# Performance work log

Measured on AMD Instinct MI355X. Metric: run time of the kernel, lower is better.

The kernel has to match this reference:

```python
import jax, jax.numpy as jnp
import numpy as np

B, C, H, W = 16, 512, 32, 32
GROUPS = 8
EPS = 1e-5


def setup_inputs() -> dict:
    key = jax.random.key(0)
    ks = jax.random.split(key, 7)
    s = 1.0 / np.sqrt(C)
    return {
        "x": jax.random.normal(ks[0], (B, C, H, W), dtype=jnp.float32),
        "gamma": jnp.ones((C,), dtype=jnp.float32),
        "beta": jnp.zeros((C,), dtype=jnp.float32),
        "w_qkv": jax.random.normal(ks[1], (3 * C, C), dtype=jnp.float32) * s,
        "b_qkv": jnp.zeros((3 * C,), dtype=jnp.float32),
        "w_proj": jax.random.normal(ks[2], (C, C), dtype=jnp.float32) * s,
        "b_proj": jnp.zeros((C,), dtype=jnp.float32),
    }


def group_norm(x, gamma, beta):
    b, c, h, w = x.shape
    xg = x.reshape(b, GROUPS, c // GROUPS, h, w)
    mean = xg.mean(axis=(2, 3, 4), keepdims=True)
    var = xg.var(axis=(2, 3, 4), keepdims=True)
    xn = ((xg - mean) * jax.lax.rsqrt(var + EPS)).reshape(b, c, h, w)
    return xn * gamma[None, :, None, None] + beta[None, :, None, None]


def reference(x, gamma, beta, w_qkv, b_qkv, w_proj, b_proj):
    b, c, h, w = x.shape
    n = h * w
    hn = group_norm(x, gamma, beta)
    # 1x1 conv == channel matmul: [3C, C] x [B, C, N] -> [B, 3C, N]
    qkv = jnp.einsum('oc,bcn->bon', w_qkv, hn.reshape(b, c, n)) + b_qkv[None, :, None]
    q, k, v = jnp.split(qkv, 3, axis=1)  # each [B, C, N]
    scale = c ** (-0.5)
    # scores [B, N, N]: q^T k
    attn = jax.nn.softmax(jnp.einsum('bcn,bcm->bnm', q, k) * scale, axis=-1)
    out = jnp.einsum('bnm,bcm->bcn', attn, v)  # [B, C, N]
    proj = jnp.einsum('oc,bcn->bon', w_proj, out) + b_proj[None, :, None]
    return x + proj.reshape(b, c, h, w)
```

## Files before the change

### kernel.cpp

```cpp
#include <hip/hip_runtime.h>


#define BATCH 16
#define CCH 512
#define NSP 1024
#define EPSV 1e-5f
#define BK 32
#define HT 4096

typedef short bf16x8 __attribute__((ext_vector_type(8)));
typedef float f32x4 __attribute__((ext_vector_type(4)));

__device__ __forceinline__ unsigned short f2bf(float f) {
    unsigned int u = __float_as_uint(f);
    u += 0x7FFF + ((u >> 16) & 1);
    return (unsigned short)(u >> 16);
}

__device__ __forceinline__ void glds16(const void* g, void* l) {
    __builtin_amdgcn_global_load_lds(
        (const __attribute__((address_space(1))) unsigned int*)g,
        (__attribute__((address_space(3))) unsigned int*)l, 16, 0, 0);
}

#define MEMF asm volatile("" ::: "memory")
#define VMW(n) asm volatile("s_waitcnt vmcnt(" #n ")" ::: "memory")

#define XCD_MAP(GX_LOG2, PER, xv, yv, bv)                 \
    const int lin_ = blockIdx.x;                          \
    const int xcd_ = lin_ & 7;                            \
    int slot_ = lin_ >> 3;                                \
    const int hi_ = (slot_ >= (PER)) ? 1 : 0;             \
    const int bv = xcd_ + 8 * hi_;                        \
    slot_ -= hi_ * (PER);                                 \
    const int xv = slot_ & ((1 << (GX_LOG2)) - 1);        \
    const int yv = slot_ >> (GX_LOG2);

__device__ __forceinline__ void gemm128_dbuf(
    const unsigned short* __restrict__ Ag, const unsigned short* __restrict__ Bg,
    int astr, int bstr, int ktot, short* L, f32x4* acc) {
    const int t = threadIdx.x;
    const int w = t >> 6, lane = t & 63;
    const int wr = (w >> 1) * 64, wc = (w & 1) * 64;
    const int fr = lane & 15;
    const int fsw = (((lane >> 4) ^ (fr & 3)) * 8);
    const int r0 = t >> 2;
    const int kc = (((t & 3) ^ (r0 & 3)) * 8);
    const unsigned short* Ap0 = Ag + (size_t)r0 * astr + kc;
    const unsigned short* Ap1 = Ag + (size_t)(r0 + 64) * astr + kc;
    const unsigned short* Bp0 = Bg + (size_t)r0 * bstr + kc;
    const unsigned short* Bp1 = Bg + (size_t)(r0 + 64) * bstr + kc;
    short* lw = L + w * 512;

#define STG(bf, kk) do {                                  \
    short* aw_ = lw + (bf) * (4 * HT);                    \
    short* bw_ = aw_ + 2 * HT;                            \
    glds16(Ap0 + (kk), aw_);                              \
    glds16(Ap1 + (kk), aw_ + 2048);                       \
    glds16(Ap0 + (kk) + 32, aw_ + HT);                    \
    glds16(Ap1 + (kk) + 32, aw_ + HT + 2048);             \
    glds16(Bp0 + (kk), bw_);                              \
    glds16(Bp1 + (kk), bw_ + 2048);                       \
    glds16(Bp0 + (kk) + 32, bw_ + HT);                    \
    glds16(Bp1 + (kk) + 32, bw_ + HT + 2048);             \
  } while (0)

#define CMP(bf) do {                                                        \
    _Pragma("unroll")                                                       \
    for (int h = 0; h < 2; h++) {                                           \
        const short* Ab_ = L + (bf) * (4 * HT) + h * HT;                    \
        const short* Bb_ = Ab_ + 2 * HT;                                    \
        bf16x8 af[4], bfr[4];                                               \
        _Pragma("unroll")                                                   \
        for (int mi = 0; mi < 4; mi++)                                      \
            af[mi] = *(const bf16x8*)(Ab_ + (wr + mi * 16 + fr) * BK + fsw);\
        _Pragma("unroll")                                                   \
        for (int ni = 0; ni < 4; ni++)                                      \
            bfr[ni] = *(const bf16x8*)(Bb_ + (wc + ni * 16 + fr) * BK + fsw);\
        _Pragma("unroll")                                                   \
        for (int mi = 0; mi < 4; mi++)                                      \
            _Pragma("unroll")                                               \
            for (int ni = 0; ni < 4; ni++)                                  \
                acc[mi * 4 + ni] = __builtin_amdgcn_mfma_f32_16x16x32_bf16( \
                    af[mi], bfr[ni], acc[mi * 4 + ni], 0, 0, 0);            \
    } } while (0)

    STG(0, 0);
    for (int k0 = 0; k0 < ktot; k0 += 128) {
        STG(1, k0 + 64);
        VMW(8);
        MEMF; __builtin_amdgcn_s_barrier();
        CMP(0);
        MEMF; __builtin_amdgcn_s_barrier();
        const int kb = (k0 + 128 < ktot) ? k0 + 128 : 0;
        STG(0, kb);
        VMW(8);
        MEMF; __builtin_amdgcn_s_barrier();
        CMP(1);
        MEMF; __builtin_amdgcn_s_barrier();
    }
    VMW(0);
#undef STG
#undef CMP
}

__device__ __forceinline__ void gemm128_sb(
    const unsigned short* __restrict__ Ag, const unsigned short* __restrict__ Bg,
    int astr, int bstr, int ktot, short* Al, short* Bl, f32x4* acc) {
    const int t = threadIdx.x;
    const int w = t >> 6, lane = t & 63;
    const int wr = (w >> 1) * 64, wc = (w & 1) * 64;
    const int fr = lane & 15;
    const int fsw = (((lane >> 4) ^ (fr & 3)) * 8);
    const int r0 = t >> 2;
    const int kc = (((t & 3) ^ (r0 & 3)) * 8);
    const unsigned short* Ap0 = Ag + (size_t)r0 * astr + kc;
    const unsigned short* Ap1 = Ag + (size_t)(r0 + 64) * astr + kc;
    const unsigned short* Bp0 = Bg + (size_t)r0 * bstr + kc;
    const unsigned short* Bp1 = Bg + (size_t)(r0 + 64) * bstr + kc;
    short* Alw = Al + w * 512;
    short* Blw = Bl + w * 512;
    for (int k0 = 0; k0 < ktot; k0 += 64) {
        glds16(Ap0 + k0, Alw);
        glds16(Ap1 + k0, Alw + 2048);
        glds16(Ap0 + k0 + 32, Alw + HT);
        glds16(Ap1 + k0 + 32, Alw + HT + 2048);
        glds16(Bp0 + k0, Blw);
        glds16(Bp1 + k0, Blw + 2048);
        glds16(Bp0 + k0 + 32, Blw + HT);
        glds16(Bp1 + k0 + 32, Blw + HT + 2048);
        __syncthreads();
#pragma unroll
        for (int h = 0; h < 2; h++) {
            const short* Ab = Al + h * HT;
            const short* Bb = Bl + h * HT;
            bf16x8 af[4], bfr[4];
#pragma unroll
            for (int mi = 0; mi < 4; mi++)
                af[mi] = *(const bf16x8*)(Ab + (wr + mi * 16 + fr) * BK + fsw);
#pragma unroll
            for (int ni = 0; ni < 4; ni++)
                bfr[ni] = *(const bf16x8*)(Bb + (wc + ni * 16 + fr) * BK + fsw);
#pragma unroll
            for (int mi = 0; mi < 4; mi++)
#pragma unroll
                for (int ni = 0; ni < 4; ni++)
                    acc[mi * 4 + ni] = __builtin_amdgcn_mfma_f32_16x16x32_bf16(
                        af[mi], bfr[ni], acc[mi * 4 + ni], 0, 0, 0);
        }
        __syncthreads();
    }
}

#define EPI_SETUP()                                          \
    const int t = threadIdx.x, lane = t & 63, w = t >> 6;    \
    const int wr = (w >> 1) * 64, wc = (w & 1) * 64;         \
    const int fr = lane & 15, rr0 = (lane >> 4) * 4;

#define ACC_INIT(acc)                                        \
    f32x4 acc[16];                                           \
    _Pragma("unroll") for (int i = 0; i < 16; i++)           \
        acc[i] = (f32x4){0.f, 0.f, 0.f, 0.f};

__global__ __launch_bounds__(256) void setup_k(
    const float* __restrict__ x, float* __restrict__ stats,
    const float* __restrict__ wa, unsigned short* __restrict__ oa, int na4,
    const float* __restrict__ wb, unsigned short* __restrict__ ob, int nb4,
    float* __restrict__ Lsum, const float* __restrict__ bqv,
    unsigned short* __restrict__ wv_t, float* __restrict__ puv) {
    const int t = threadIdx.x;
    const int bx = blockIdx.x;
    __shared__ float rs[4], rq[4];
    __shared__ __align__(16) unsigned short Tt[64 * 72];
    if (bx < 128) {
        const int bg = bx;
        const float4* xp = (const float4*)(x + (size_t)bg * 65536);
        float s = 0.f, q = 0.f;
#pragma unroll
        for (int i = 0; i < 64; i++) {
            float4 v = xp[t + i * 256];
            s += v.x + v.y + v.z + v.w;
            q += v.x * v.x + v.y * v.y + v.z * v.z + v.w * v.w;
        }
#pragma unroll
        for (int off = 32; off; off >>= 1) {
            s += __shfl_down(s, off);
            q += __shfl_down(q, off);
        }
        const int wave = t >> 6, lane = t & 63;
        if (lane == 0) { rs[wave] = s; rq[wave] = q; }
        __syncthreads();
        if (t == 0) {
            float S = rs[0] + rs[1] + rs[2] + rs[3];
            float Q = rq[0] + rq[1] + rq[2] + rq[3];
            const float inv = 1.f / 65536.f;
            float mean = S * inv;
            float var = Q * inv - mean * mean;
            stats[bg * 2] = mean;
            stats[bg * 2 + 1] = rsqrtf(var + EPSV);
        }
    } else if (bx < 896) {
        int i = (bx - 128) * 256 + t;
        const float* src;
        unsigned short* dst;
        int j;
        if (i < na4) { src = wa; dst = oa; j = i; }
        else { j = i - na4; if (j >= nb4) return; src = wb; dst = ob; }
        float4 v = ((const float4*)src)[j];
        ushort4 o;
        o.x = f2bf(v.x); o.y = f2bf(v.y); o.z = f2bf(v.z); o.w = f2bf(v.w);
        ((ushort4*)dst)[j] = o;
    } else if (bx < 912) {
        int i = (bx - 896) * 256 + t;
        ((float4*)Lsum)[i] = (float4){0.f, 0.f, 0.f, 0.f};
    } else if (bx < 976) {
        const int r = bx - 912;
        const float* src = wa + (size_t)2 * 512 * 512;
        const int to = (r >> 3) * 64, tc = (r & 7) * 64;
        const int ol = t >> 2, cs = t & 3;
#pragma unroll
        for (int j = 0; j < 4; j++) {
            float4 v = *(const float4*)(src + (size_t)(to + ol) * 512 + tc + cs * 16 + j * 4);
            int c = cs * 16 + j * 4;
            Tt[(c + 0) * 72 + ol] = f2bf(v.x);
            Tt[(c + 1) * 72 + ol] = f2bf(v.y);
            Tt[(c + 2) * 72 + ol] = f2bf(v.z);
            Tt[(c + 3) * 72 + ol] = f2bf(v.w);
        }
        __syncthreads();
        const int cl = t >> 2, os = t & 3;
        unsigned short* d = wv_t + (size_t)(tc + cl) * 512 + to + os * 16;
        const unsigned short* s2 = Tt + cl * 72 + os * 16;
        *(uint4*)d = *(const uint4*)s2;
        *(uint4*)(d + 8) = *(const uint4*)(s2 + 8);
    } else {
        const int o = (bx - 976) * 256 + t;
        const float* wr_ = wb + (size_t)o * 512;
        const float* bv = bqv + 1024;
        float s = 0.f;
        for (int vv = 0; vv < 512; vv += 4) {
            s += wr_[vv] * bv[vv] + wr_[vv + 1] * bv[vv + 1]
               + wr_[vv + 2] * bv[vv + 2] + wr_[vv + 3] * bv[vv + 3];
        }
        puv[o] = s;
    }
}

__global__ __launch_bounds__(256) void gn_tr_k(
    const float* __restrict__ x, const float* __restrict__ gamma,
    const float* __restrict__ beta, const float* __restrict__ stats,
    unsigned short* __restrict__ hn_t,
    const unsigned short* __restrict__ wp_bf, const unsigned short* __restrict__ wv_t,
    unsigned short* __restrict__ wpv_bf) {
    __shared__ __align__(16) short SM[4 * HT];
    const int lin = blockIdx.x;
    const int t = threadIdx.x;
    if (lin < 16) {
        const int ot = (lin >> 2) * 128, ct2 = (lin & 3) * 128;
        ACC_INIT(acc);
        gemm128_sb(wp_bf + (size_t)ot * 512, wv_t + (size_t)ct2 * 512,
                   512, 512, 512, SM, SM + 2 * HT, acc);
        EPI_SETUP();
#pragma unroll
        for (int ni = 0; ni < 4; ni++) {
            int col = ct2 + wc + ni * 16 + fr;
#pragma unroll
            for (int mi = 0; mi < 4; mi++) {
                int row = ot + wr + mi * 16 + rr0;
#pragma unroll
                for (int r = 0; r < 4; r++)
                    wpv_bf[(size_t)(row + r) * 512 + col] = f2bf(acc[mi * 4 + ni][r]);
            }
        }
        return;
    }
    const int l2 = lin - 16;
    const int nt = l2 & 15, ct = (l2 >> 4) & 7, b = l2 >> 7;
    unsigned short* T = (unsigned short*)SM;
    const float mean = stats[(b * 8 + ct) * 2];
    const float rstd = stats[(b * 8 + ct) * 2 + 1];
    const int cl = t >> 2, nc = t & 3;
    const int c = ct * 64 + cl;
    const float ga = gamma[c] * rstd;
    const float be = beta[c] - mean * ga;
    const float4* xp = (const float4*)(x + ((size_t)b * CCH + c) * NSP + nt * 64);
#pragma unroll
    for (int j = 0; j < 4; j++) {
        float4 v = xp[nc * 4 + j];
        int n = nc * 16 + j * 4;
        T[(n + 0) * 72 + cl] = f2bf(v.x * ga + be);
        T[(n + 1) * 72 + cl] = f2bf(v.y * ga + be);
        T[(n + 2) * 72 + cl] = f2bf(v.z * ga + be);
        T[(n + 3) * 72 + cl] = f2bf(v.w * ga + be);
    }
    __syncthreads();
    const int nl = t >> 2, cc = t & 3;
    unsigned short* dst = hn_t + ((size_t)b * NSP + nt * 64 + nl) * CCH + ct * 64 + cc * 16;
    const unsigned short* src = T + nl * 72 + cc * 16;
    *(uint4*)dst = *(const uint4*)src;
    *(uint4*)(dst + 8) = *(const uint4*)(src + 8);
}

__global__ __launch_bounds__(256) void gemm_qku_k(
    const unsigned short* __restrict__ hn_t, const unsigned short* __restrict__ wq,
    const float* __restrict__ bq, const unsigned short* __restrict__ wpv_bf,
    const float* __restrict__ puv, unsigned short* __restrict__ QKt,
    unsigned short* __restrict__ Ub) {
    __shared__ __align__(16) short L[8 * HT];
    XCD_MAP(3, 96, xb, y, b);
    const int ntc = xb * 128;
    ACC_INIT(acc);
    if (y < 8) {
        const int mt = y * 128;
        gemm128_dbuf(hn_t + ((size_t)b * NSP + mt) * CCH,
                     wq + (size_t)ntc * CCH, CCH, CCH, CCH, L, acc);
        unsigned short* Ob = QKt + (size_t)b * NSP * 1024;
        EPI_SETUP();
#pragma unroll
        for (int ni = 0; ni < 4; ni++) {
            int col = ntc + wc + ni * 16 + fr;
            float bias = bq[col];
#pragma unroll
            for (int mi = 0; mi < 4; mi++) {
                int row = mt + wr + mi * 16 + rr0;
#pragma unroll
                for (int r = 0; r < 4; r++)
                    Ob[(size_t)(row + r) * 1024 + col] = f2bf(acc[mi * 4 + ni][r] + bias);
            }
        }
    } else {
        const int mt = (y - 8) * 128;
        gemm128_dbuf(wpv_bf + (size_t)mt * 512,
                     hn_t + ((size_t)b * NSP + ntc) * CCH, 512, CCH, 512, L, acc);
        unsigned short* Ob = Ub + (size_t)b * CCH * NSP;
        EPI_SETUP();
#pragma unroll
        for (int mi = 0; mi < 4; mi++) {
            int row = mt + wr + mi * 16 + rr0;
#pragma unroll
            for (int r = 0; r < 4; r++) {
                float bias = puv[row + r];
#pragma unroll
                for (int ni = 0; ni < 4; ni++) {
                    int col = ntc + wc + ni * 16 + fr;
                    Ob[(size_t)(row + r) * NSP + col] = f2bf(acc[mi * 4 + ni][r] + bias);
                }
            }
        }
    }
}

__global__ __launch_bounds__(256) void gemm_scores_k(
    const unsigned short* __restrict__ QKt, unsigned short* __restrict__ expS,
    float* __restrict__ Lsum) {
    __shared__ __align__(16) short L[8 * HT];
    XCD_MAP(3, 64, xb, yb, b);
    const int nt = xb * 128, mt = yb * 128;
    const unsigned short* base = QKt + (size_t)b * NSP * 1024;
    ACC_INIT(acc);
    gemm128_dbuf(base + (size_t)mt * 1024, base + (size_t)nt * 1024 + 512,
                 1024, 1024, 512, L, acc);
    unsigned short* Ob = expS + (size_t)b * NSP * NSP;
    float* Ls = Lsum + (size_t)b * NSP;
    const float scale = 0.044194173824159216f;
    EPI_SETUP();
#pragma unroll
    for (int mi = 0; mi < 4; mi++) {
#pragma unroll
        for (int r = 0; r < 4; r++) {
            const int row = mt + wr + mi * 16 + rr0 + r;
            float rs = 0.f;
#pragma unroll
            for (int ni = 0; ni < 4; ni++) {
                int col = nt + wc + ni * 16 + fr;
                float e = __expf(acc[mi * 4 + ni][r] * scale);
                Ob[(size_t)row * NSP + col] = f2bf(e);
                rs += e;
            }
            rs += __shfl_xor(rs, 1);
            rs += __shfl_xor(rs, 2);
            rs += __shfl_xor(rs, 4);
            rs += __shfl_xor(rs, 8);
            if (fr == 0) atomicAdd(&Ls[row], rs);
        }
    }
}

__global__ __launch_bounds__(256) void gemm_pu_k(
    const unsigned short* __restrict__ Ub, const unsigned short* __restrict__ expS,
    const float* __restrict__ Lsum, const float* __restrict__ x,
    const float* __restrict__ bp, float* __restrict__ out) {
    __shared__ __align__(16) short L[8 * HT];
    XCD_MAP(3, 32, xb, yb, b);
    const int nt = xb * 128, ot = yb * 128;
    ACC_INIT(acc);
    gemm128_dbuf(Ub + ((size_t)b * CCH + ot) * NSP,
                 expS + ((size_t)b * NSP + nt) * NSP, NSP, NSP, NSP, L, acc);
    const float* Ls = Lsum + (size_t)b * NSP;
    const size_t bbase = (size_t)b * CCH * NSP;
    EPI_SETUP();
#pragma unroll
    for (int ni = 0; ni < 4; ni++) {
        int col = nt + wc + ni * 16 + fr;
        float invl = __builtin_amdgcn_rcpf(Ls[col]);
#pragma unroll
        for (int mi = 0; mi < 4; mi++) {
            int row = ot + wr + mi * 16 + rr0;
#pragma unroll
            for (int r = 0; r < 4; r++) {
                size_t idx = bbase + (size_t)(row + r) * NSP + col;
                out[idx] = x[idx] + bp[row + r] + acc[mi * 4 + ni][r] * invl;
            }
        }
    }
}

extern "C" void kernel_launch(void* const* d_in, const int* in_sizes, int n_in,
                              void* d_out, int out_size, void* d_ws, size_t ws_size,
                              hipStream_t stream) {
    const float* x = (const float*)d_in[0];
    const float* gamma = (const float*)d_in[1];
    const float* beta = (const float*)d_in[2];
    const float* w_qkv = (const float*)d_in[3];
    const float* b_qkv = (const float*)d_in[4];
    const float* w_proj = (const float*)d_in[5];
    const float* b_proj = (const float*)d_in[6];
    float* out = (float*)d_out;

    char* ws = (char*)d_ws;
    const size_t MB = 1048576;
    const size_t KB = 1024;
    unsigned short* wqkv_bf = (unsigned short*)ws;
    unsigned short* wproj_bf = (unsigned short*)(ws + 1572864);
    float* stats = (float*)(ws + 2 * MB);
    float* Lsum = (float*)(ws + 2 * MB + 64 * KB);
    float* puv = (float*)(ws + 2 * MB + 128 * KB);
    unsigned short* wv_t = (unsigned short*)(ws + 2 * MB + 256 * KB);
    unsigned short* wpv_bf = (unsigned short*)(ws + 3 * MB);
    unsigned short* hn_t = (unsigned short*)(ws + 4 * MB);
    unsigned short* QKt = (unsigned short*)(ws + 24 * MB);
    unsigned short* Ub = (unsigned short*)(ws + 60 * MB);
    unsigned short* expS = (unsigned short*)(ws + 80 * MB);

    setup_k<<<978, 256, 0, stream>>>(x, stats, w_qkv, wqkv_bf, 131072,
                                     w_proj, wproj_bf, 65536, Lsum, b_qkv,
                                     wv_t, puv);
    gn_tr_k<<<2064, 256, 0, stream>>>(x, gamma, beta, stats, hn_t,
                                      wproj_bf, wv_t, wpv_bf);
    gemm_qku_k<<<1536, 256, 0, stream>>>(hn_t, wqkv_bf, b_qkv, wpv_bf, puv,
                                         QKt, Ub);
    gemm_scores_k<<<1024, 256, 0, stream>>>(QKt, expS, Lsum);
    gemm_pu_k<<<512, 256, 0, stream>>>(Ub, expS, Lsum, x, b_proj, out);
}
```

Measured before the change: 204.6 us.

## Fold Wq^T Wk into one matrix so scores skip separate Q and K projections

Precomputes the 512x512 product Wk^T Wq in bf16 inside gn_tr_k. The main GEMM then produces a single T1 = hn·(Wq^T Wk) instead of separate Q and K, which cuts the qkv GEMM from 1536 to 1024 tiles. The scores GEMM now multiplies T1 by the normalized input directly, and the bias cross-terms are added back as per-row and per-column vectors plus a constant in the exp epilogue. The group-norm statistics pass is also split into 512 partial-sum blocks for more parallelism. The cost is extra weight-prep work, atomics for the bias vectors, and a different bf16 rounding path for the combined matrix.

```diff
diff --git a/kernel.cpp b/kernel.cpp
--- a/kernel.cpp
+++ b/kernel.cpp
@@ -15,6 +15,10 @@
     unsigned int u = __float_as_uint(f);
     u += 0x7FFF + ((u >> 16) & 1);
     return (unsigned short)(u >> 16);
+}
+
+__device__ __forceinline__ float bf2f(unsigned short h) {
+    return __uint_as_float(((unsigned int)h) << 16);
 }
 
 __device__ __forceinline__ void glds16(const void* g, void* l) {
@@ -163,44 +167,41 @@
         acc[i] = (f32x4){0.f, 0.f, 0.f, 0.f};
 
 __global__ __launch_bounds__(256) void setup_k(
-    const float* __restrict__ x, float* __restrict__ stats,
+    const float* __restrict__ x, float* __restrict__ sp,
     const float* __restrict__ wa, unsigned short* __restrict__ oa, int na4,
     const float* __restrict__ wb, unsigned short* __restrict__ ob, int nb4,
     float* __restrict__ Lsum, const float* __restrict__ bqv,
-    unsigned short* __restrict__ wv_t, float* __restrict__ puv) {
+    unsigned short* __restrict__ wv_t, unsigned short* __restrict__ wq_t,
+    unsigned short* __restrict__ wk_t, float* __restrict__ puv,
+    float* __restrict__ wu, float* __restrict__ wv_b, float* __restrict__ c0p) {
     const int t = threadIdx.x;
     const int bx = blockIdx.x;
     __shared__ float rs[4], rq[4];
     __shared__ __align__(16) unsigned short Tt[64 * 72];
-    if (bx < 128) {
-        const int bg = bx;
-        const float4* xp = (const float4*)(x + (size_t)bg * 65536);
-        float s = 0.f, q = 0.f;
-#pragma unroll
-        for (int i = 0; i < 64; i++) {
+    if (bx < 512) {
+        const int bg = bx >> 2, q = bx & 3;
+        const float4* xp = (const float4*)(x + (size_t)bg * 65536 + q * 16384);
+        float s = 0.f, qq = 0.f;
+#pragma unroll
+        for (int i = 0; i < 16; i++) {
             float4 v = xp[t + i * 256];
             s += v.x + v.y + v.z + v.w;
-            q += v.x * v.x + v.y * v.y + v.z * v.z + v.w * v.w;
+            qq += v.x * v.x + v.y * v.y + v.z * v.z + v.w * v.w;
         }
 #pragma unroll
         for (int off = 32; off; off >>= 1) {
             s += __shfl_down(s, off);
-            q += __shfl_down(q, off);
+            qq += __shfl_down(qq, off);
         }
         const int wave = t >> 6, lane = t & 63;
-        if (lane == 0) { rs[wave] = s; rq[wave] = q; }
+        if (lane == 0) { rs[wave] = s; rq[wave] = qq; }
         __syncthreads();
         if (t == 0) {
-            float S = rs[0] + rs[1] + rs[2] + rs[3];
-            float Q = rq[0] + rq[1] + rq[2] + rq[3];
-            const float inv = 1.f / 65536.f;
-            float mean = S * inv;
-            float var = Q * inv - mean * mean;
-            stats[bg * 2] = mean;
-            stats[bg * 2 + 1] = rsqrtf(var + EPSV);
-        }
-    } else if (bx < 896) {
-        int i = (bx - 128) * 256 + t;
+            sp[bx * 2] = rs[0] + rs[1] + rs[2] + rs[3];
+            sp[bx * 2 + 1] = rq[0] + rq[1] + rq[2] + rq[3];
+        }
+    } else if (bx < 1280) {
+        int i = (bx - 512) * 256 + t;
         const float* src;
         unsigned short* dst;
         int j;
@@ -210,13 +211,16 @@
         ushort4 o;
         o.x = f2bf(v.x); o.y = f2bf(v.y); o.z = f2bf(v.z); o.w = f2bf(v.w);
         ((ushort4*)dst)[j] = o;
-    } else if (bx < 912) {
-        int i = (bx - 896) * 256 + t;
+    } else if (bx < 1328) {
+        int i = (bx - 1280) * 256 + t;
         ((float4*)Lsum)[i] = (float4){0.f, 0.f, 0.f, 0.f};
-    } else if (bx < 976) {
-        const int r = bx - 912;
-        const float* src = wa + (size_t)2 * 512 * 512;
-        const int to = (r >> 3) * 64, tc = (r & 7) * 64;
+    } else if (bx < 1520) {
+        const int r = bx - 1328;
+        const int sel = r >> 6;
+        const int wrow = (sel == 0) ? 2 : (sel - 1);
+        const float* src = wa + (size_t)wrow * 512 * 512;
+        unsigned short* dst = (sel == 0) ? wv_t : ((sel == 1) ? wq_t : wk_t);
+        const int to = ((r & 63) >> 3) * 64, tc = ((r & 63) & 7) * 64;
         const int ol = t >> 2, cs = t & 3;
 #pragma unroll
         for (int j = 0; j < 4; j++) {
@@ -229,12 +233,12 @@
         }
         __syncthreads();
         const int cl = t >> 2, os = t & 3;
-        unsigned short* d = wv_t + (size_t)(tc + cl) * 512 + to + os * 16;
+        unsigned short* d = dst + (size_t)(tc + cl) * 512 + to + os * 16;
         const unsigned short* s2 = Tt + cl * 72 + os * 16;
         *(uint4*)d = *(const uint4*)s2;
         *(uint4*)(d + 8) = *(const uint4*)(s2 + 8);
-    } else {
-        const int o = (bx - 976) * 256 + t;
+    } else if (bx < 1522) {
+        const int o = (bx - 1520) * 256 + t;
         const float* wr_ = wb + (size_t)o * 512;
         const float* bv = bqv + 1024;
         float s = 0.f;
@@ -243,15 +247,35 @@
                + wr_[vv + 2] * bv[vv + 2] + wr_[vv + 3] * bv[vv + 3];
         }
         puv[o] = s;
+    } else if (bx < 1526) {
+        const int r = bx - 1522;
+        const int isv = r >> 1;
+        const int c = (r & 1) * 256 + t;
+        const float* src = wa + (size_t)isv * 512 * 512;
+        const float* bsr = bqv + (isv ? 0 : 512);
+        float s = 0.f;
+        for (int o = 0; o < 512; o++) s += src[(size_t)o * 512 + c] * bsr[o];
+        (isv ? wv_b : wu)[c] = s;
+    } else {
+        float s = bqv[t] * bqv[512 + t] + bqv[256 + t] * bqv[768 + t];
+#pragma unroll
+        for (int off = 32; off; off >>= 1) s += __shfl_down(s, off);
+        if ((t & 63) == 0) rs[t >> 6] = s;
+        __syncthreads();
+        if (t == 0) c0p[0] = rs[0] + rs[1] + rs[2] + rs[3];
     }
 }
 
 __global__ __launch_bounds__(256) void gn_tr_k(
     const float* __restrict__ x, const float* __restrict__ gamma,
-    const float* __restrict__ beta, const float* __restrict__ stats,
+    const float* __restrict__ beta, const float* __restrict__ sp,
     unsigned short* __restrict__ hn_t,
     const unsigned short* __restrict__ wp_bf, const unsigned short* __restrict__ wv_t,
-    unsigned short* __restrict__ wpv_bf) {
+    unsigned short* __restrict__ wpv_bf,
+    const unsigned short* __restrict__ wk_t, const unsigned short* __restrict__ wq_t,
+    unsigned short* __restrict__ wqkb,
+    const float* __restrict__ wu, const float* __restrict__ wv_b,
+    float* __restrict__ u, float* __restrict__ v) {
     __shared__ __align__(16) short SM[4 * HT];
     const int lin = blockIdx.x;
     const int t = threadIdx.x;
@@ -274,11 +298,39 @@
         }
         return;
     }
-    const int l2 = lin - 16;
+    if (lin < 32) {
+        const int r2 = lin - 16;
+        const int jt = (r2 >> 2) * 128, ct2 = (r2 & 3) * 128;
+        ACC_INIT(acc);
+        gemm128_sb(wk_t + (size_t)jt * 512, wq_t + (size_t)ct2 * 512,
+                   512, 512, 512, SM, SM + 2 * HT, acc);
+        EPI_SETUP();
+#pragma unroll
+        for (int ni = 0; ni < 4; ni++) {
+            int col = ct2 + wc + ni * 16 + fr;
+#pragma unroll
+            for (int mi = 0; mi < 4; mi++) {
+                int row = jt + wr + mi * 16 + rr0;
+#pragma unroll
+                for (int r = 0; r < 4; r++)
+                    wqkb[(size_t)(row + r) * 512 + col] = f2bf(acc[mi * 4 + ni][r]);
+            }
+        }
+        return;
+    }
+    const int l2 = lin - 32;
     const int nt = l2 & 15, ct = (l2 >> 4) & 7, b = l2 >> 7;
     unsigned short* T = (unsigned short*)SM;
-    const float mean = stats[(b * 8 + ct) * 2];
-    const float rstd = stats[(b * 8 + ct) * 2 + 1];
+    const int bg = b * 8 + ct;
+    float S = 0.f, Q = 0.f;
+#pragma unroll
+    for (int qq = 0; qq < 4; qq++) {
+        S += sp[(bg * 4 + qq) * 2];
+        Q += sp[(bg * 4 + qq) * 2 + 1];
+    }
+    const float inv = 1.f / 65536.f;
+    const float mean = S * inv;
+    const float rstd = rsqrtf(Q * inv - mean * mean + EPSV);
     const int cl = t >> 2, nc = t & 3;
     const int c = ct * 64 + cl;
     const float ga = gamma[c] * rstd;
@@ -286,12 +338,12 @@
     const float4* xp = (const float4*)(x + ((size_t)b * CCH + c) * NSP + nt * 64);
 #pragma unroll
     for (int j = 0; j < 4; j++) {
-        float4 v = xp[nc * 4 + j];
+        float4 vx = xp[nc * 4 + j];
         int n = nc * 16 + j * 4;
-        T[(n + 0) * 72 + cl] = f2bf(v.x * ga + be);
-        T[(n + 1) * 72 + cl] = f2bf(v.y * ga + be);
-        T[(n + 2) * 72 + cl] = f2bf(v.z * ga + be);
-        T[(n + 3) * 72 + cl] = f2bf(v.w * ga + be);
+        T[(n + 0) * 72 + cl] = f2bf(vx.x * ga + be);
+        T[(n + 1) * 72 + cl] = f2bf(vx.y * ga + be);
+        T[(n + 2) * 72 + cl] = f2bf(vx.z * ga + be);
+        T[(n + 3) * 72 + cl] = f2bf(vx.w * ga + be);
     }
     __syncthreads();
     const int nl = t >> 2, cc = t & 3;
@@ -299,44 +351,60 @@
     const unsigned short* src = T + nl * 72 + cc * 16;
     *(uint4*)dst = *(const uint4*)src;
     *(uint4*)(dst + 8) = *(const uint4*)(src + 8);
+    float pu = 0.f, pv = 0.f;
+    const int cbase = ct * 64 + cc * 16;
+#pragma unroll
+    for (int j = 0; j < 16; j++) {
+        float hv = bf2f(src[j]);
+        pu += hv * wu[cbase + j];
+        pv += hv * wv_b[cbase + j];
+    }
+    pu += __shfl_xor(pu, 1); pu += __shfl_xor(pu, 2);
+    pv += __shfl_xor(pv, 1); pv += __shfl_xor(pv, 2);
+    if (cc == 0) {
+        atomicAdd(&u[(size_t)b * NSP + nt * 64 + nl], pu);
+        atomicAdd(&v[(size_t)b * NSP + nt * 64 + nl], pv);
+    }
 }
 
 __global__ __launch_bounds__(256) void gemm_qku_k(
-    const unsigned short* __restrict__ hn_t, const unsigned short* __restrict__ wq,
-    const float* __restrict__ bq, const unsigned short* __restrict__ wpv_bf,
-    const float* __restrict__ puv, unsigned short* __restrict__ QKt,
-    unsigned short* __restrict__ Ub) {
+    const unsigned short* __restrict__ hn_t, const unsigned short* __restrict__ wqkb,
+    const unsigned short* __restrict__ wpv_bf, const float* __restrict__ puv,
+    unsigned short* __restrict__ T1, unsigned short* __restrict__ Ub) {
     __shared__ __align__(16) short L[8 * HT];
-    XCD_MAP(3, 96, xb, y, b);
-    const int ntc = xb * 128;
+    const int lin = blockIdx.x, xcd = lin & 7;
+    int slot = lin >> 3;
+    const int hi = (slot >= 64) ? 1 : 0;
+    const int b = xcd + 8 * hi;
+    slot -= hi * 64;
     ACC_INIT(acc);
-    if (y < 8) {
-        const int mt = y * 128;
+    if (slot < 32) {
+        const int mt = (slot >> 2) * 128, jt = (slot & 3) * 128;
         gemm128_dbuf(hn_t + ((size_t)b * NSP + mt) * CCH,
-                     wq + (size_t)ntc * CCH, CCH, CCH, CCH, L, acc);
-        unsigned short* Ob = QKt + (size_t)b * NSP * 1024;
+                     wqkb + (size_t)jt * 512, CCH, 512, CCH, L, acc);
+        unsigned short* Ob = T1 + (size_t)b * NSP * 512;
         EPI_SETUP();
 #pragma unroll
         for (int ni = 0; ni < 4; ni++) {
-            int col = ntc + wc + ni * 16 + fr;
-            float bias = bq[col];
+            int col = jt + wc + ni * 16 + fr;
 #pragma unroll
             for (int mi = 0; mi < 4; mi++) {
                 int row = mt + wr + mi * 16 + rr0;
 #pragma unroll
                 for (int r = 0; r < 4; r++)
-                    Ob[(size_t)(row + r) * 1024 + col] = f2bf(acc[mi * 4 + ni][r] + bias);
+                    Ob[(size_t)(row + r) * 512 + col] = f2bf(acc[mi * 4 + ni][r]);
             }
         }
     } else {
-        const int mt = (y - 8) * 128;
-        gemm128_dbuf(wpv_bf + (size_t)mt * 512,
+        const int s2 = slot - 32;
+        const int ot = (s2 >> 3) * 128, ntc = (s2 & 7) * 128;
+        gemm128_dbuf(wpv_bf + (size_t)ot * 512,
                      hn_t + ((size_t)b * NSP + ntc) * CCH, 512, CCH, 512, L, acc);
         unsigned short* Ob = Ub + (size_t)b * CCH * NSP;
         EPI_SETUP();
 #pragma unroll
         for (int mi = 0; mi < 4; mi++) {
-            int row = mt + wr + mi * 16 + rr0;
+            int row = ot + wr + mi * 16 + rr0;
 #pragma unroll
             for (int r = 0; r < 4; r++) {
                 float bias = puv[row + r];
@@ -351,17 +419,21 @@
 }
 
 __global__ __launch_bounds__(256) void gemm_scores_k(
-    const unsigned short* __restrict__ QKt, unsigned short* __restrict__ expS,
-    float* __restrict__ Lsum) {
+    const unsigned short* __restrict__ T1, const unsigned short* __restrict__ hn_t,
+    unsigned short* __restrict__ expS, float* __restrict__ Lsum,
+    const float* __restrict__ u, const float* __restrict__ v,
+    const float* __restrict__ c0p) {
     __shared__ __align__(16) short L[8 * HT];
     XCD_MAP(3, 64, xb, yb, b);
     const int nt = xb * 128, mt = yb * 128;
-    const unsigned short* base = QKt + (size_t)b * NSP * 1024;
     ACC_INIT(acc);
-    gemm128_dbuf(base + (size_t)mt * 1024, base + (size_t)nt * 1024 + 512,
-                 1024, 1024, 512, L, acc);
+    gemm128_dbuf(T1 + ((size_t)b * NSP + mt) * 512,
+                 hn_t + ((size_t)b * NSP + nt) * CCH, 512, CCH, 512, L, acc);
     unsigned short* Ob = expS + (size_t)b * NSP * NSP;
     float* Ls = Lsum + (size_t)b * NSP;
+    const float* ua = u + (size_t)b * NSP;
+    const float* va = v + (size_t)b * NSP;
+    const float c0v = c0p[0];
     const float scale = 0.044194173824159216f;
     EPI_SETUP();
 #pragma unroll
@@ -369,11 +441,12 @@
 #pragma unroll
         for (int r = 0; r < 4; r++) {
             const int row = mt + wr + mi * 16 + rr0 + r;
+            const float ur = ua[row] + c0v;
             float rs = 0.f;
 #pragma unroll
             for (int ni = 0; ni < 4; ni++) {
                 int col = nt + wc + ni * 16 + fr;
-                float e = __expf(acc[mi * 4 + ni][r] * scale);
+                float e = __expf((acc[mi * 4 + ni][r] + ur + va[col]) * scale);
                 Ob[(size_t)row * NSP + col] = f2bf(e);
                 rs += e;
             }
@@ -432,23 +505,31 @@
     const size_t KB = 1024;
     unsigned short* wqkv_bf = (unsigned short*)ws;
     unsigned short* wproj_bf = (unsigned short*)(ws + 1572864);
-    float* stats = (float*)(ws + 2 * MB);
+    float* sp = (float*)(ws + 2 * MB);
     float* Lsum = (float*)(ws + 2 * MB + 64 * KB);
-    float* puv = (float*)(ws + 2 * MB + 128 * KB);
-    unsigned short* wv_t = (unsigned short*)(ws + 2 * MB + 256 * KB);
-    unsigned short* wpv_bf = (unsigned short*)(ws + 3 * MB);
+    float* u = (float*)(ws + 2 * MB + 128 * KB);
+    float* v = (float*)(ws + 2 * MB + 192 * KB);
+    float* puv = (float*)(ws + 2 * MB + 256 * KB);
+    float* wu = (float*)(ws + 2 * MB + 260 * KB);
+    float* wv_b = (float*)(ws + 2 * MB + 264 * KB);
+    float* c0p = (float*)(ws + 2 * MB + 268 * KB);
+    unsigned short* wv_t = (unsigned short*)(ws + 2 * MB + 512 * KB);
+    unsigned short* wq_t = (unsigned short*)(ws + 3 * MB);
+    unsigned short* wk_t = (unsigned short*)(ws + 3 * MB + 512 * KB);
     unsigned short* hn_t = (unsigned short*)(ws + 4 * MB);
-    unsigned short* QKt = (unsigned short*)(ws + 24 * MB);
+    unsigned short* T1 = (unsigned short*)(ws + 24 * MB);
     unsigned short* Ub = (unsigned short*)(ws + 60 * MB);
     unsigned short* expS = (unsigned short*)(ws + 80 * MB);
-
-    setup_k<<<978, 256, 0, stream>>>(x, stats, w_qkv, wqkv_bf, 131072,
-                                     w_proj, wproj_bf, 65536, Lsum, b_qkv,
-                                     wv_t, puv);
-    gn_tr_k<<<2064, 256, 0, stream>>>(x, gamma, beta, stats, hn_t,
-                                      wproj_bf, wv_t, wpv_bf);
-    gemm_qku_k<<<1536, 256, 0, stream>>>(hn_t, wqkv_bf, b_qkv, wpv_bf, puv,
-                                         QKt, Ub);
-    gemm_scores_k<<<1024, 256, 0, stream>>>(QKt, expS, Lsum);
+    unsigned short* wpv_bf = (unsigned short*)(ws + 114 * MB);
+    unsigned short* wqkb = (unsigned short*)(ws + 115 * MB);
+
+    setup_k<<<1527, 256, 0, stream>>>(x, sp, w_qkv, wqkv_bf, 131072,
+                                      w_proj, wproj_bf, 65536, Lsum, b_qkv,
+                                      wv_t, wq_t, wk_t, puv, wu, wv_b, c0p);
+    gn_tr_k<<<2080, 256, 0, stream>>>(x, gamma, beta, sp, hn_t,
+                                      wproj_bf, wv_t, wpv_bf,
+                                      wk_t, wq_t, wqkb, wu, wv_b, u, v);
+    gemm_qku_k<<<1024, 256, 0, stream>>>(hn_t, wqkb, wpv_bf, puv, T1, Ub);
+    gemm_scores_k<<<1024, 256, 0, stream>>>(T1, hn_t, expS, Lsum, u, v, c0p);
     gemm_pu_k<<<512, 256, 0, stream>>>(Ub, expS, Lsum, x, b_proj, out);
 }
```

After: 208.2 us. No clear change (+1.8%).

## Split GroupNorm stats into partial blocks and halve final GEMM tile height

Applied to the files above, without the earlier changes.

The stats reduction now uses four blocks per group, each writing partial sum and sum-of-squares; gn_tr_k combines them into mean and rstd. The final P·U GEMM switches from 128x128 tiles to 64x128 tiles with a new double-buffered 64-row GEMM routine, doubling its grid from 512 to 1024 blocks. Both changes aim to raise parallelism and CU occupancy on small grids. The cost is less data reuse per tile in the final GEMM and an extra small reduction in the normalization kernel.

```diff
diff --git a/kernel.cpp b/kernel.cpp
--- a/kernel.cpp
+++ b/kernel.cpp
@@ -95,6 +95,70 @@
         const int kb = (k0 + 128 < ktot) ? k0 + 128 : 0;
         STG(0, kb);
         VMW(8);
+        MEMF; __builtin_amdgcn_s_barrier();
+        CMP(1);
+        MEMF; __builtin_amdgcn_s_barrier();
+    }
+    VMW(0);
+#undef STG
+#undef CMP
+}
+
+__device__ __forceinline__ void gemm64_d64(
+    const unsigned short* __restrict__ Ag, const unsigned short* __restrict__ Bg,
+    int astr, int bstr, int ktot, short* L, f32x4* acc) {
+    const int t = threadIdx.x;
+    const int w = t >> 6, lane = t & 63;
+    const int wc = w * 32;
+    const int fr = lane & 15;
+    const int fsw = (((lane >> 4) ^ (fr & 3)) * 8);
+    const int r0 = t >> 2;
+    const int kc = (((t & 3) ^ (r0 & 3)) * 8);
+    const unsigned short* Ap0 = Ag + (size_t)r0 * astr + kc;
+    const unsigned short* Bp0 = Bg + (size_t)r0 * bstr + kc;
+    const unsigned short* Bp1 = Bg + (size_t)(r0 + 64) * bstr + kc;
+    short* lw = L + w * 512;
+
+#define STG(bf, kk) do {                                  \
+    short* p_ = lw + (bf) * 12288;                        \
+    glds16(Ap0 + (kk), p_);                               \
+    glds16(Ap0 + (kk) + 32, p_ + 2048);                   \
+    glds16(Bp0 + (kk), p_ + 4096);                        \
+    glds16(Bp1 + (kk), p_ + 6144);                        \
+    glds16(Bp0 + (kk) + 32, p_ + 8192);                   \
+    glds16(Bp1 + (kk) + 32, p_ + 10240);                  \
+  } while (0)
+
+#define CMP(bf) do {                                                        \
+    _Pragma("unroll")                                                       \
+    for (int h = 0; h < 2; h++) {                                           \
+        const short* Ab_ = L + (bf) * 12288 + h * 2048;                     \
+        const short* Bb_ = L + (bf) * 12288 + 4096 + h * 4096;              \
+        bf16x8 af[4], bfr[2];                                               \
+        _Pragma("unroll")                                                   \
+        for (int mi = 0; mi < 4; mi++)                                      \
+            af[mi] = *(const bf16x8*)(Ab_ + (mi * 16 + fr) * 32 + fsw);     \
+        _Pragma("unroll")                                                   \
+        for (int ni = 0; ni < 2; ni++)                                      \
+            bfr[ni] = *(const bf16x8*)(Bb_ + (wc + ni * 16 + fr) * 32 + fsw);\
+        _Pragma("unroll")                                                   \
+        for (int mi = 0; mi < 4; mi++)                                      \
+            _Pragma("unroll")                                               \
+            for (int ni = 0; ni < 2; ni++)                                  \
+                acc[mi * 2 + ni] = __builtin_amdgcn_mfma_f32_16x16x32_bf16( \
+                    af[mi], bfr[ni], acc[mi * 2 + ni], 0, 0, 0);            \
+    } } while (0)
+
+    STG(0, 0);
+    for (int k0 = 0; k0 < ktot; k0 += 128) {
+        STG(1, k0 + 64);
+        VMW(6);
+        MEMF; __builtin_amdgcn_s_barrier();
+        CMP(0);
+        MEMF; __builtin_amdgcn_s_barrier();
+        const int kb = (k0 + 128 < ktot) ? k0 + 128 : 0;
+        STG(0, kb);
+        VMW(6);
         MEMF; __builtin_amdgcn_s_barrier();
         CMP(1);
         MEMF; __builtin_amdgcn_s_barrier();
@@ -163,7 +227,7 @@
         acc[i] = (f32x4){0.f, 0.f, 0.f, 0.f};
 
 __global__ __launch_bounds__(256) void setup_k(
-    const float* __restrict__ x, float* __restrict__ stats,
+    const float* __restrict__ x, float* __restrict__ sp,
     const float* __restrict__ wa, unsigned short* __restrict__ oa, int na4,
     const float* __restrict__ wb, unsigned short* __restrict__ ob, int nb4,
     float* __restrict__ Lsum, const float* __restrict__ bqv,
@@ -172,35 +236,30 @@
     const int bx = blockIdx.x;
     __shared__ float rs[4], rq[4];
     __shared__ __align__(16) unsigned short Tt[64 * 72];
-    if (bx < 128) {
-        const int bg = bx;
-        const float4* xp = (const float4*)(x + (size_t)bg * 65536);
-        float s = 0.f, q = 0.f;
-#pragma unroll
-        for (int i = 0; i < 64; i++) {
+    if (bx < 512) {
+        const int bg = bx >> 2, q = bx & 3;
+        const float4* xp = (const float4*)(x + (size_t)bg * 65536 + q * 16384);
+        float s = 0.f, qq = 0.f;
+#pragma unroll
+        for (int i = 0; i < 16; i++) {
             float4 v = xp[t + i * 256];
             s += v.x + v.y + v.z + v.w;
-            q += v.x * v.x + v.y * v.y + v.z * v.z + v.w * v.w;
+            qq += v.x * v.x + v.y * v.y + v.z * v.z + v.w * v.w;
         }
 #pragma unroll
         for (int off = 32; off; off >>= 1) {
             s += __shfl_down(s, off);
-            q += __shfl_down(q, off);
+            qq += __shfl_down(qq, off);
         }
         const int wave = t >> 6, lane = t & 63;
-        if (lane == 0) { rs[wave] = s; rq[wave] = q; }
+        if (lane == 0) { rs[wave] = s; rq[wave] = qq; }
         __syncthreads();
         if (t == 0) {
-            float S = rs[0] + rs[1] + rs[2] + rs[3];
-            float Q = rq[0] + rq[1] + rq[2] + rq[3];
-            const float inv = 1.f / 65536.f;
-            float mean = S * inv;
-            float var = Q * inv - mean * mean;
-            stats[bg * 2] = mean;
-            stats[bg * 2 + 1] = rsqrtf(var + EPSV);
-        }
-    } else if (bx < 896) {
-        int i = (bx - 128) * 256 + t;
+            sp[bx * 2] = rs[0] + rs[1] + rs[2] + rs[3];
+            sp[bx * 2 + 1] = rq[0] + rq[1] + rq[2] + rq[3];
+        }
+    } else if (bx < 1280) {
+        int i = (bx - 512) * 256 + t;
         const float* src;
         unsigned short* dst;
         int j;
@@ -210,11 +269,11 @@
         ushort4 o;
         o.x = f2bf(v.x); o.y = f2bf(v.y); o.z = f2bf(v.z); o.w = f2bf(v.w);
         ((ushort4*)dst)[j] = o;
-    } else if (bx < 912) {
-        int i = (bx - 896) * 256 + t;
+    } else if (bx < 1296) {
+        int i = (bx - 1280) * 256 + t;
         ((float4*)Lsum)[i] = (float4){0.f, 0.f, 0.f, 0.f};
-    } else if (bx < 976) {
-        const int r = bx - 912;
+    } else if (bx < 1360) {
+        const int r = bx - 1296;
         const float* src = wa + (size_t)2 * 512 * 512;
         const int to = (r >> 3) * 64, tc = (r & 7) * 64;
         const int ol = t >> 2, cs = t & 3;
@@ -234,7 +293,7 @@
         *(uint4*)d = *(const uint4*)s2;
         *(uint4*)(d + 8) = *(const uint4*)(s2 + 8);
     } else {
-        const int o = (bx - 976) * 256 + t;
+        const int o = (bx - 1360) * 256 + t;
         const float* wr_ = wb + (size_t)o * 512;
         const float* bv = bqv + 1024;
         float s = 0.f;
@@ -248,7 +307,7 @@
 
 __global__ __launch_bounds__(256) void gn_tr_k(
     const float* __restrict__ x, const float* __restrict__ gamma,
-    const float* __restrict__ beta, const float* __restrict__ stats,
+    const float* __restrict__ beta, const float* __restrict__ sp,
     unsigned short* __restrict__ hn_t,
     const unsigned short* __restrict__ wp_bf, const unsigned short* __restrict__ wv_t,
     unsigned short* __restrict__ wpv_bf) {
@@ -277,8 +336,16 @@
     const int l2 = lin - 16;
     const int nt = l2 & 15, ct = (l2 >> 4) & 7, b = l2 >> 7;
     unsigned short* T = (unsigned short*)SM;
-    const float mean = stats[(b * 8 + ct) * 2];
-    const float rstd = stats[(b * 8 + ct) * 2 + 1];
+    const int bg = b * 8 + ct;
+    float S = 0.f, Q = 0.f;
+#pragma unroll
+    for (int qq = 0; qq < 4; qq++) {
+        S += sp[(bg * 4 + qq) * 2];
+        Q += sp[(bg * 4 + qq) * 2 + 1];
+    }
+    const float inv = 1.f / 65536.f;
+    const float mean = S * inv;
+    const float rstd = rsqrtf(Q * inv - mean * mean + EPSV);
     const int cl = t >> 2, nc = t & 3;
     const int c = ct * 64 + cl;
     const float ga = gamma[c] * rstd;
@@ -390,26 +457,30 @@
     const unsigned short* __restrict__ Ub, const unsigned short* __restrict__ expS,
     const float* __restrict__ Lsum, const float* __restrict__ x,
     const float* __restrict__ bp, float* __restrict__ out) {
-    __shared__ __align__(16) short L[8 * HT];
-    XCD_MAP(3, 32, xb, yb, b);
-    const int nt = xb * 128, ot = yb * 128;
-    ACC_INIT(acc);
-    gemm128_dbuf(Ub + ((size_t)b * CCH + ot) * NSP,
-                 expS + ((size_t)b * NSP + nt) * NSP, NSP, NSP, NSP, L, acc);
+    __shared__ __align__(16) short L[24576];
+    XCD_MAP(3, 64, xb, yb, b);
+    const int nt = xb * 128, ot = yb * 64;
+    f32x4 acc[8];
+#pragma unroll
+    for (int i = 0; i < 8; i++) acc[i] = (f32x4){0.f, 0.f, 0.f, 0.f};
+    gemm64_d64(Ub + ((size_t)b * CCH + ot) * NSP,
+               expS + ((size_t)b * NSP + nt) * NSP, NSP, NSP, NSP, L, acc);
     const float* Ls = Lsum + (size_t)b * NSP;
     const size_t bbase = (size_t)b * CCH * NSP;
-    EPI_SETUP();
-#pragma unroll
-    for (int ni = 0; ni < 4; ni++) {
+    const int t = threadIdx.x, lane = t & 63, w = t >> 6;
+    const int fr = lane & 15, rr0 = (lane >> 4) * 4;
+    const int wc = w * 32;
+#pragma unroll
+    for (int ni = 0; ni < 2; ni++) {
         int col = nt + wc + ni * 16 + fr;
         float invl = __builtin_amdgcn_rcpf(Ls[col]);
 #pragma unroll
         for (int mi = 0; mi < 4; mi++) {
-            int row = ot + wr + mi * 16 + rr0;
+            int row = ot + mi * 16 + rr0;
 #pragma unroll
             for (int r = 0; r < 4; r++) {
                 size_t idx = bbase + (size_t)(row + r) * NSP + col;
-                out[idx] = x[idx] + bp[row + r] + acc[mi * 4 + ni][r] * invl;
+                out[idx] = x[idx] + bp[row + r] + acc[mi * 2 + ni][r] * invl;
             }
         }
     }
@@ -432,7 +503,7 @@
     const size_t KB = 1024;
     unsigned short* wqkv_bf = (unsigned short*)ws;
     unsigned short* wproj_bf = (unsigned short*)(ws + 1572864);
-    float* stats = (float*)(ws + 2 * MB);
+    float* sp = (float*)(ws + 2 * MB);
     float* Lsum = (float*)(ws + 2 * MB + 64 * KB);
     float* puv = (float*)(ws + 2 * MB + 128 * KB);
     unsigned short* wv_t = (unsigned short*)(ws + 2 * MB + 256 * KB);
@@ -442,13 +513,13 @@
     unsigned short* Ub = (unsigned short*)(ws + 60 * MB);
     unsigned short* expS = (unsigned short*)(ws + 80 * MB);
 
-    setup_k<<<978, 256, 0, stream>>>(x, stats, w_qkv, wqkv_bf, 131072,
-                                     w_proj, wproj_bf, 65536, Lsum, b_qkv,
-                                     wv_t, puv);
-    gn_tr_k<<<2064, 256, 0, stream>>>(x, gamma, beta, stats, hn_t,
+    setup_k<<<1362, 256, 0, stream>>>(x, sp, w_qkv, wqkv_bf, 131072,
+                                      w_proj, wproj_bf, 65536, Lsum, b_qkv,
+                                      wv_t, puv);
+    gn_tr_k<<<2064, 256, 0, stream>>>(x, gamma, beta, sp, hn_t,
                                       wproj_bf, wv_t, wpv_bf);
     gemm_qku_k<<<1536, 256, 0, stream>>>(hn_t, wqkv_bf, b_qkv, wpv_bf, puv,
                                          QKt, Ub);
     gemm_scores_k<<<1024, 256, 0, stream>>>(QKt, expS, Lsum);
-    gemm_pu_k<<<512, 256, 0, stream>>>(Ub, expS, Lsum, x, b_proj, out);
-}
+    gemm_pu_k<<<1024, 256, 0, stream>>>(Ub, expS, Lsum, x, b_proj, out);
+}
```

Result: slower. 214.4 us (+4.8%).
